# Optimization experiments

Measured on AMD Instinct MI355X. Metric: run time of the kernel, lower is better.

Reference implementation:

```python
import jax, jax.numpy as jnp
import numpy as np

BASIS_ORDER = 7  # basis_dim = 8 (Chebyshev T_0..T_7 of tanh(x))


def chebyshev_basis(x, order=BASIS_ORDER):
    """x: [batch, in] -> [batch, in, order+1] Chebyshev basis on tanh(x)."""
    xt = jnp.tanh(x)
    terms = [jnp.ones_like(xt), xt]
    for _ in range(2, order + 1):
        terms.append(2.0 * xt * terms[-1] - terms[-2])
    return jnp.stack(terms[: order + 1], axis=-1)


def setup_inputs() -> dict:
    key = jax.random.key(0)
    k1, k2, k3 = jax.random.split(key, 3)
    batch, in_f, out_f, K = 4096, 1024, 1024, BASIS_ORDER + 1
    x = jax.random.normal(k1, (batch, in_f), dtype=jnp.float32)
    # Kaiming-uniform-ish init scale
    bound = 1.0 / np.sqrt(in_f * K)
    weights = jax.random.uniform(k2, (out_f, in_f, K), dtype=jnp.float32,
                                 minval=-bound, maxval=bound)
    bias_param = jax.random.uniform(k3, (out_f,), dtype=jnp.float32,
                                    minval=-bound, maxval=bound)
    return {"x": x, "weights": weights, "bias_param": bias_param}


def reference(x, weights, bias_param):
    # basis: [b, i, k]; weights: [o, i, k] -> out[b, o] = sum_{i,k} basis*W
    basis = chebyshev_basis(x)  # [batch, in, K]
    out = jnp.einsum('bik,oik->bo', basis, weights)
    return out + bias_param
```

## Files before the change

### kernel.cpp

```cpp
#include <hip/hip_runtime.h>
#include <hip/hip_bf16.h>

#define MD 4096
#define ND 1024
#define KD 8192
#define IN_F 1024

typedef __bf16 bf16x8 __attribute__((ext_vector_type(8)));
typedef float f32x4 __attribute__((ext_vector_type(4)));

#define N_BASIS (MD * IN_F)
#define N_CONV ((ND * KD) / 8)

__global__ __launch_bounds__(256) void prep_kernel(
    const float* __restrict__ x, const float* __restrict__ w,
    __bf16* __restrict__ A, __bf16* __restrict__ B) {
  int i = blockIdx.x * blockDim.x + threadIdx.x;
  if (i < N_BASIS) {
    float t = tanhf(x[i]);
    float two_t = 2.0f * t;
    float T0 = 1.0f;
    float T1 = t;
    float T2 = two_t * T1 - T0;
    float T3 = two_t * T2 - T1;
    float T4 = two_t * T3 - T2;
    float T5 = two_t * T4 - T3;
    float T6 = two_t * T5 - T4;
    float T7 = two_t * T6 - T5;
    bf16x8 v;
    v[0] = (__bf16)T0; v[1] = (__bf16)T1; v[2] = (__bf16)T2; v[3] = (__bf16)T3;
    v[4] = (__bf16)T4; v[5] = (__bf16)T5; v[6] = (__bf16)T6; v[7] = (__bf16)T7;
    *(bf16x8*)(A + (size_t)i * 8) = v;
  } else if (i < N_BASIS + N_CONV) {
    int j = i - N_BASIS;
    const float4* p = (const float4*)(w + (size_t)j * 8);
    float4 a = p[0], b = p[1];
    bf16x8 v;
    v[0] = (__bf16)a.x; v[1] = (__bf16)a.y; v[2] = (__bf16)a.z; v[3] = (__bf16)a.w;
    v[4] = (__bf16)b.x; v[5] = (__bf16)b.y; v[6] = (__bf16)b.z; v[7] = (__bf16)b.w;
    *(bf16x8*)(B + (size_t)j * 8) = v;
  }
}

#define BM 64
#define BN 128
#define BK 64

__global__ __launch_bounds__(256) void gemm_bias(
    const __bf16* __restrict__ A, const __bf16* __restrict__ B,
    const float* __restrict__ bias, float* __restrict__ C) {
  __shared__ __align__(16) __bf16 As[BM * BK];
  __shared__ __align__(16) __bf16 Bs[BN * BK];

  const int tid = threadIdx.x;
  const int wave = tid >> 6;
  const int lane = tid & 63;

  const int b = blockIdx.x;
  const int xcd = b & 7;
  const int j = b >> 3;
  const int nt = j & 7;
  const int mloc = j >> 3;
  const int n0 = nt * BN;
  const int m0 = (xcd * 8 + mloc) * BM;

  const int wm = wave >> 1;
  const int wn = wave & 1;

  const int ar = lane >> 3;
  const int swz_col = ((lane & 7) ^ ar) * 8;
  const __bf16* gA = A + (size_t)(m0 + wave * 16 + ar) * KD + swz_col;
  const __bf16* gB = B + (size_t)(n0 + wave * 32 + ar) * KD + swz_col;
  const __bf16* lA = As + (wave * 16) * BK;
  const __bf16* lB = Bs + (wave * 32) * BK;

  f32x4 acc[2][4];
#pragma unroll
  for (int i = 0; i < 2; i++)
#pragma unroll
    for (int jj = 0; jj < 4; jj++) acc[i][jj] = (f32x4){0.f, 0.f, 0.f, 0.f};

  const int fr = lane & 15;
  const int fr7 = fr & 7;
  const int qk = lane >> 4;

  for (int kt = 0; kt < KD; kt += BK) {
#pragma unroll
    for (int jj = 0; jj < 2; jj++)
      __builtin_amdgcn_global_load_lds(
          (const __attribute__((address_space(1))) void*)(gA + kt + (size_t)jj * 8 * KD),
          (__attribute__((address_space(3))) void*)(lA + jj * 8 * BK), 16, 0, 0);
#pragma unroll
    for (int jj = 0; jj < 4; jj++)
      __builtin_amdgcn_global_load_lds(
          (const __attribute__((address_space(1))) void*)(gB + kt + (size_t)jj * 8 * KD),
          (__attribute__((address_space(3))) void*)(lB + jj * 8 * BK), 16, 0, 0);
    __syncthreads();

#pragma unroll
    for (int s = 0; s < 2; s++) {
      const int pa = ((s * 4 + qk) ^ fr7) * 8;
      bf16x8 af[2], bfr[4];
#pragma unroll
      for (int mi = 0; mi < 2; mi++)
        af[mi] = *(const bf16x8*)&As[(wm * 32 + mi * 16 + fr) * BK + pa];
#pragma unroll
      for (int ni = 0; ni < 4; ni++)
        bfr[ni] = *(const bf16x8*)&Bs[(wn * 64 + ni * 16 + fr) * BK + pa];
#pragma unroll
      for (int mi = 0; mi < 2; mi++)
#pragma unroll
        for (int ni = 0; ni < 4; ni++)
          acc[mi][ni] = __builtin_amdgcn_mfma_f32_16x16x32_bf16(
              af[mi], bfr[ni], acc[mi][ni], 0, 0, 0);
    }
    __syncthreads();
  }

  const int col0 = n0 + wn * 64;
  const int row0 = m0 + wm * 32 + (lane >> 4) * 4;
#pragma unroll
  for (int ni = 0; ni < 4; ni++) {
    int col = col0 + ni * 16 + (lane & 15);
    float bv = bias[col];
#pragma unroll
    for (int mi = 0; mi < 2; mi++) {
      int row = row0 + mi * 16;
#pragma unroll
      for (int r = 0; r < 4; r++)
        C[(size_t)(row + r) * ND + col] = acc[mi][ni][r] + bv;
    }
  }
}

extern "C" void kernel_launch(void* const* d_in, const int* in_sizes, int n_in,
                              void* d_out, int out_size, void* d_ws, size_t ws_size,
                              hipStream_t stream) {
  const float* x = (const float*)d_in[0];
  const float* w = (const float*)d_in[1];
  const float* bias = (const float*)d_in[2];
  float* out = (float*)d_out;

  __bf16* Abf = (__bf16*)d_ws;
  __bf16* Bbf = (__bf16*)((char*)d_ws + (size_t)MD * KD * 2);

  {
    int n = N_BASIS + N_CONV;
    prep_kernel<<<(n + 255) / 256, 256, 0, stream>>>(x, w, Abf, Bbf);
  }
  {
    gemm_bias<<<512, 256, 0, stream>>>(Abf, Bbf, bias, out);
  }
}
```

Before: 187.8 us.

## Enlarge GEMM tile to 128x128 and add triple-buffered async LDS pipeline

Doubles the M tile to 128 so each wave computes a 64x64 sub-tile, halving the grid to 256 blocks. It also replaces the single-buffered load/sync/compute loop with a three-stage LDS ring, where global_load_lds for the next tile is issued before waiting on the current one via vmcnt. The aim is to hide global load latency and raise MFMA work per LDS byte. In exchange there are more registers and more LDS per block, and 256 blocks may underfill the 256 CUs, leaving little latency hiding through occupancy. Synchronisation now depends on a single barrier per iteration with hand-tuned waitcnt values.

```diff
diff --git a/kernel.cpp b/kernel.cpp
--- a/kernel.cpp
+++ b/kernel.cpp
@@ -42,15 +42,17 @@
   }
 }
 
-#define BM 64
+#define BM 128
 #define BN 128
 #define BK 64
+#define NT (KD / BK)
+#define TSZ (BM * BK)
 
-__global__ __launch_bounds__(256) void gemm_bias(
+__global__ __launch_bounds__(256, 1) void gemm_bias(
     const __bf16* __restrict__ A, const __bf16* __restrict__ B,
     const float* __restrict__ bias, float* __restrict__ C) {
-  __shared__ __align__(16) __bf16 As[BM * BK];
-  __shared__ __align__(16) __bf16 Bs[BN * BK];
+  __shared__ __align__(16) __bf16 As[3][TSZ];
+  __shared__ __align__(16) __bf16 Bs[3][TSZ];
 
   const int tid = threadIdx.x;
   const int wave = tid >> 6;
@@ -62,21 +64,20 @@
   const int nt = j & 7;
   const int mloc = j >> 3;
   const int n0 = nt * BN;
-  const int m0 = (xcd * 8 + mloc) * BM;
+  const int m0 = (xcd * 4 + mloc) * BM;
 
   const int wm = wave >> 1;
   const int wn = wave & 1;
 
   const int ar = lane >> 3;
   const int swz_col = ((lane & 7) ^ ar) * 8;
-  const __bf16* gA = A + (size_t)(m0 + wave * 16 + ar) * KD + swz_col;
+  const __bf16* gA = A + (size_t)(m0 + wave * 32 + ar) * KD + swz_col;
   const __bf16* gB = B + (size_t)(n0 + wave * 32 + ar) * KD + swz_col;
-  const __bf16* lA = As + (wave * 16) * BK;
-  const __bf16* lB = Bs + (wave * 32) * BK;
+  const int loff = wave * 32 * BK;
 
-  f32x4 acc[2][4];
+  f32x4 acc[4][4];
 #pragma unroll
-  for (int i = 0; i < 2; i++)
+  for (int i = 0; i < 4; i++)
 #pragma unroll
     for (int jj = 0; jj < 4; jj++) acc[i][jj] = (f32x4){0.f, 0.f, 0.f, 0.f};
 
@@ -84,47 +85,69 @@
   const int fr7 = fr & 7;
   const int qk = lane >> 4;
 
-  for (int kt = 0; kt < KD; kt += BK) {
 #pragma unroll
-    for (int jj = 0; jj < 2; jj++)
-      __builtin_amdgcn_global_load_lds(
-          (const __attribute__((address_space(1))) void*)(gA + kt + (size_t)jj * 8 * KD),
-          (__attribute__((address_space(3))) void*)(lA + jj * 8 * BK), 16, 0, 0);
-#pragma unroll
-    for (int jj = 0; jj < 4; jj++)
-      __builtin_amdgcn_global_load_lds(
-          (const __attribute__((address_space(1))) void*)(gB + kt + (size_t)jj * 8 * KD),
-          (__attribute__((address_space(3))) void*)(lB + jj * 8 * BK), 16, 0, 0);
-    __syncthreads();
-
-#pragma unroll
-    for (int s = 0; s < 2; s++) {
-      const int pa = ((s * 4 + qk) ^ fr7) * 8;
-      bf16x8 af[2], bfr[4];
-#pragma unroll
-      for (int mi = 0; mi < 2; mi++)
-        af[mi] = *(const bf16x8*)&As[(wm * 32 + mi * 16 + fr) * BK + pa];
-#pragma unroll
-      for (int ni = 0; ni < 4; ni++)
-        bfr[ni] = *(const bf16x8*)&Bs[(wn * 64 + ni * 16 + fr) * BK + pa];
-#pragma unroll
-      for (int mi = 0; mi < 2; mi++)
-#pragma unroll
-        for (int ni = 0; ni < 4; ni++)
-          acc[mi][ni] = __builtin_amdgcn_mfma_f32_16x16x32_bf16(
-              af[mi], bfr[ni], acc[mi][ni], 0, 0, 0);
-    }
-    __syncthreads();
+  for (int jj = 0; jj < 4; jj++) {
+    __builtin_amdgcn_global_load_lds(
+        (const __attribute__((address_space(1))) void*)(gA + (size_t)jj * 8 * KD),
+        (__attribute__((address_space(3))) void*)(&As[0][loff + jj * 8 * BK]), 16, 0, 0);
+    __builtin_amdgcn_global_load_lds(
+        (const __attribute__((address_space(1))) void*)(gB + (size_t)jj * 8 * KD),
+        (__attribute__((address_space(3))) void*)(&Bs[0][loff + jj * 8 * BK]), 16, 0, 0);
   }
 
+#define ITER(T, CUR, NXT, WAIT)                                                \
+  do {                                                                         \
+    const int tn = ((T) + 1 < NT) ? (T) + 1 : 0;                               \
+    _Pragma("unroll") for (int jj = 0; jj < 4; jj++) {                         \
+      __builtin_amdgcn_global_load_lds(                                        \
+          (const __attribute__((address_space(1))) void*)(                     \
+              gA + (size_t)tn * BK + (size_t)jj * 8 * KD),                     \
+          (__attribute__((address_space(3))) void*)(                           \
+              &As[NXT][loff + jj * 8 * BK]), 16, 0, 0);                        \
+      __builtin_amdgcn_global_load_lds(                                        \
+          (const __attribute__((address_space(1))) void*)(                     \
+              gB + (size_t)tn * BK + (size_t)jj * 8 * KD),                     \
+          (__attribute__((address_space(3))) void*)(                           \
+              &Bs[NXT][loff + jj * 8 * BK]), 16, 0, 0);                        \
+    }                                                                          \
+    asm volatile(WAIT ::: "memory");                                           \
+    __builtin_amdgcn_s_barrier();                                              \
+    asm volatile("" ::: "memory");                                             \
+    _Pragma("unroll") for (int s = 0; s < 2; s++) {                            \
+      const int pa = ((s * 4 + qk) ^ fr7) * 8;                                 \
+      bf16x8 af[4], bfr[4];                                                    \
+      _Pragma("unroll") for (int mi = 0; mi < 4; mi++)                         \
+          af[mi] = *(const bf16x8*)&As[CUR][(wm * 64 + mi * 16 + fr) * BK + pa]; \
+      _Pragma("unroll") for (int ni = 0; ni < 4; ni++)                         \
+          bfr[ni] = *(const bf16x8*)&Bs[CUR][(wn * 64 + ni * 16 + fr) * BK + pa]; \
+      _Pragma("unroll") for (int mi = 0; mi < 4; mi++)                         \
+          _Pragma("unroll") for (int ni = 0; ni < 4; ni++)                     \
+              acc[mi][ni] = __builtin_amdgcn_mfma_f32_16x16x32_bf16(           \
+                  af[mi], bfr[ni], acc[mi][ni], 0, 0, 0);                      \
+    }                                                                          \
+  } while (0)
+
+  ITER(0, 0, 1, "s_waitcnt vmcnt(0)");
+  ITER(1, 1, 2, "s_waitcnt vmcnt(8)");
+  ITER(2, 2, 0, "s_waitcnt vmcnt(8)");
+#pragma unroll 1
+  for (int t0 = 3; t0 < 126; t0 += 3) {
+    ITER(t0, 0, 1, "s_waitcnt vmcnt(8)");
+    ITER(t0 + 1, 1, 2, "s_waitcnt vmcnt(8)");
+    ITER(t0 + 2, 2, 0, "s_waitcnt vmcnt(8)");
+  }
+  ITER(126, 0, 1, "s_waitcnt vmcnt(8)");
+  ITER(127, 1, 2, "s_waitcnt vmcnt(8)");
+#undef ITER
+
   const int col0 = n0 + wn * 64;
-  const int row0 = m0 + wm * 32 + (lane >> 4) * 4;
+  const int row0 = m0 + wm * 64 + qk * 4;
 #pragma unroll
   for (int ni = 0; ni < 4; ni++) {
-    int col = col0 + ni * 16 + (lane & 15);
+    int col = col0 + ni * 16 + fr;
     float bv = bias[col];
 #pragma unroll
-    for (int mi = 0; mi < 2; mi++) {
+    for (int mi = 0; mi < 4; mi++) {
       int row = row0 + mi * 16;
 #pragma unroll
       for (int r = 0; r < 4; r++)
@@ -149,6 +172,6 @@
     prep_kernel<<<(n + 255) / 256, 256, 0, stream>>>(x, w, Abf, Bbf);
   }
   {
-    gemm_bias<<<512, 256, 0, stream>>>(Abf, Bbf, bias, out);
+    gemm_bias<<<256, 256, 0, stream>>>(Abf, Bbf, bias, out);
   }
 }
```

New measurement: 183.7 us. 2.2% less time.

## Use 128x128 tiles with split-K over two halves plus reduce kernel

Applied to the files above, without the earlier changes.

Grows the GEMM block tile from 64x128 to 128x128, which raises per-wave MFMA work and data reuse from LDS. To keep 512 blocks filling the GPU, the K dimension is split in two halves: one half writes to the output with bias, the other writes to a workspace buffer. A new reduce kernel then adds the two. The cost is an extra 16MB of partial-sum traffic and one more kernel launch.

```diff
diff --git a/kernel.cpp b/kernel.cpp
--- a/kernel.cpp
+++ b/kernel.cpp
@@ -42,15 +42,19 @@
   }
 }
 
-#define BM 64
+#define BM 128
 #define BN 128
 #define BK 64
+#define KHALF 4096
+#define NTH (KHALF / BK)
+#define TSZ (BM * BK)
 
 __global__ __launch_bounds__(256) void gemm_bias(
     const __bf16* __restrict__ A, const __bf16* __restrict__ B,
-    const float* __restrict__ bias, float* __restrict__ C) {
-  __shared__ __align__(16) __bf16 As[BM * BK];
-  __shared__ __align__(16) __bf16 Bs[BN * BK];
+    const float* __restrict__ bias, float* __restrict__ C,
+    float* __restrict__ P1) {
+  __shared__ __align__(16) __bf16 As[TSZ];
+  __shared__ __align__(16) __bf16 Bs[TSZ];
 
   const int tid = threadIdx.x;
   const int wave = tid >> 6;
@@ -60,23 +64,24 @@
   const int xcd = b & 7;
   const int j = b >> 3;
   const int nt = j & 7;
-  const int mloc = j >> 3;
+  const int kh = (j >> 3) & 1;
+  const int mloc = j >> 4;
   const int n0 = nt * BN;
-  const int m0 = (xcd * 8 + mloc) * BM;
+  const int m0 = (xcd * 4 + mloc) * BM;
+  const size_t k0 = (size_t)kh * KHALF;
 
   const int wm = wave >> 1;
   const int wn = wave & 1;
 
   const int ar = lane >> 3;
   const int swz_col = ((lane & 7) ^ ar) * 8;
-  const __bf16* gA = A + (size_t)(m0 + wave * 16 + ar) * KD + swz_col;
-  const __bf16* gB = B + (size_t)(n0 + wave * 32 + ar) * KD + swz_col;
-  const __bf16* lA = As + (wave * 16) * BK;
-  const __bf16* lB = Bs + (wave * 32) * BK;
+  const __bf16* gA = A + (size_t)(m0 + wave * 32 + ar) * KD + k0 + swz_col;
+  const __bf16* gB = B + (size_t)(n0 + wave * 32 + ar) * KD + k0 + swz_col;
+  const int loff = wave * 32 * BK;
 
-  f32x4 acc[2][4];
+  f32x4 acc[4][4];
 #pragma unroll
-  for (int i = 0; i < 2; i++)
+  for (int i = 0; i < 4; i++)
 #pragma unroll
     for (int jj = 0; jj < 4; jj++) acc[i][jj] = (f32x4){0.f, 0.f, 0.f, 0.f};
 
@@ -84,31 +89,30 @@
   const int fr7 = fr & 7;
   const int qk = lane >> 4;
 
-  for (int kt = 0; kt < KD; kt += BK) {
+  for (int kt = 0; kt < KHALF; kt += BK) {
 #pragma unroll
-    for (int jj = 0; jj < 2; jj++)
+    for (int jj = 0; jj < 4; jj++) {
       __builtin_amdgcn_global_load_lds(
           (const __attribute__((address_space(1))) void*)(gA + kt + (size_t)jj * 8 * KD),
-          (__attribute__((address_space(3))) void*)(lA + jj * 8 * BK), 16, 0, 0);
-#pragma unroll
-    for (int jj = 0; jj < 4; jj++)
+          (__attribute__((address_space(3))) void*)(&As[loff + jj * 8 * BK]), 16, 0, 0);
       __builtin_amdgcn_global_load_lds(
           (const __attribute__((address_space(1))) void*)(gB + kt + (size_t)jj * 8 * KD),
-          (__attribute__((address_space(3))) void*)(lB + jj * 8 * BK), 16, 0, 0);
+          (__attribute__((address_space(3))) void*)(&Bs[loff + jj * 8 * BK]), 16, 0, 0);
+    }
     __syncthreads();
 
 #pragma unroll
     for (int s = 0; s < 2; s++) {
       const int pa = ((s * 4 + qk) ^ fr7) * 8;
-      bf16x8 af[2], bfr[4];
+      bf16x8 af[4], bfr[4];
 #pragma unroll
-      for (int mi = 0; mi < 2; mi++)
-        af[mi] = *(const bf16x8*)&As[(wm * 32 + mi * 16 + fr) * BK + pa];
+      for (int mi = 0; mi < 4; mi++)
+        af[mi] = *(const bf16x8*)&As[(wm * 64 + mi * 16 + fr) * BK + pa];
 #pragma unroll
       for (int ni = 0; ni < 4; ni++)
         bfr[ni] = *(const bf16x8*)&Bs[(wn * 64 + ni * 16 + fr) * BK + pa];
 #pragma unroll
-      for (int mi = 0; mi < 2; mi++)
+      for (int mi = 0; mi < 4; mi++)
 #pragma unroll
         for (int ni = 0; ni < 4; ni++)
           acc[mi][ni] = __builtin_amdgcn_mfma_f32_16x16x32_bf16(
@@ -117,20 +121,31 @@
     __syncthreads();
   }
 
+  float* dst = kh ? P1 : C;
   const int col0 = n0 + wn * 64;
-  const int row0 = m0 + wm * 32 + (lane >> 4) * 4;
+  const int row0 = m0 + wm * 64 + qk * 4;
 #pragma unroll
   for (int ni = 0; ni < 4; ni++) {
-    int col = col0 + ni * 16 + (lane & 15);
-    float bv = bias[col];
+    int col = col0 + ni * 16 + fr;
+    float bv = kh ? 0.0f : bias[col];
 #pragma unroll
-    for (int mi = 0; mi < 2; mi++) {
+    for (int mi = 0; mi < 4; mi++) {
       int row = row0 + mi * 16;
 #pragma unroll
       for (int r = 0; r < 4; r++)
-        C[(size_t)(row + r) * ND + col] = acc[mi][ni][r] + bv;
+        dst[(size_t)(row + r) * ND + col] = acc[mi][ni][r] + bv;
     }
   }
+}
+
+__global__ __launch_bounds__(256) void reduce_kernel(
+    float* __restrict__ C, const float* __restrict__ P1) {
+  size_t i = (size_t)blockIdx.x * blockDim.x + threadIdx.x;
+  f32x4 c = ((const f32x4*)C)[i];
+  f32x4 p = ((const f32x4*)P1)[i];
+#pragma unroll
+  for (int r = 0; r < 4; r++) c[r] += p[r];
+  ((f32x4*)C)[i] = c;
 }
 
 extern "C" void kernel_launch(void* const* d_in, const int* in_sizes, int n_in,
@@ -143,12 +158,16 @@
 
   __bf16* Abf = (__bf16*)d_ws;
   __bf16* Bbf = (__bf16*)((char*)d_ws + (size_t)MD * KD * 2);
+  float* P1 = (float*)((char*)d_ws + (size_t)MD * KD * 2 + (size_t)ND * KD * 2);
 
   {
     int n = N_BASIS + N_CONV;
     prep_kernel<<<(n + 255) / 256, 256, 0, stream>>>(x, w, Abf, Bbf);
   }
   {
-    gemm_bias<<<512, 256, 0, stream>>>(Abf, Bbf, bias, out);
+    gemm_bias<<<512, 256, 0, stream>>>(Abf, Bbf, bias, out, P1);
+  }
+  {
+    reduce_kernel<<<(MD * ND) / 4 / 256, 256, 0, stream>>>(out, P1);
   }
 }
```

New measurement: 179.0 us. 1.05x faster.
